# Optimization experiments

Hardware: AMD Instinct MI355X
Metric: run time of the kernel (lower is better)

Reference implementation:

```python
import jax, jax.numpy as jnp
import numpy as np

D_MODEL = 1024
N_HEADS = 16
D_K = D_MODEL // N_HEADS
FF_DIM = 4096
EPS = 1e-6
NEG = -1.0e9


def _layernorm(x, g, b):
    # torch: a_2 * (x - mean) / (std + eps) + b_2, std is unbiased (ddof=1)
    mean = jnp.mean(x, axis=-1, keepdims=True)
    std = jnp.std(x, axis=-1, keepdims=True, ddof=1)
    return g * (x - mean) / (std + EPS) + b


def setup_inputs() -> dict:
    key = jax.random.key(0)
    ks = jax.random.split(key, 8)
    s = 0.02
    x = jax.random.normal(ks[0], (2, 2048, D_MODEL), dtype=jnp.float32)
    mask = jnp.ones((2, 1, 1, 2048), dtype=jnp.int32)
    return {
        "x": x,
        "mask": mask,
        "wq": jax.random.normal(ks[1], (D_MODEL, D_MODEL), jnp.float32) * s,
        "wk": jax.random.normal(ks[2], (D_MODEL, D_MODEL), jnp.float32) * s,
        "wv": jax.random.normal(ks[3], (D_MODEL, D_MODEL), jnp.float32) * s,
        "wo": jax.random.normal(ks[4], (D_MODEL, D_MODEL), jnp.float32) * s,
        "bq": jnp.zeros((D_MODEL,), jnp.float32),
        "bk": jnp.zeros((D_MODEL,), jnp.float32),
        "bv": jnp.zeros((D_MODEL,), jnp.float32),
        "bo": jnp.zeros((D_MODEL,), jnp.float32),
        "w1": jax.random.normal(ks[5], (D_MODEL, FF_DIM), jnp.float32) * s,
        "b1": jnp.zeros((FF_DIM,), jnp.float32),
        "w2": jax.random.normal(ks[6], (FF_DIM, D_MODEL), jnp.float32) * s,
        "b2": jnp.zeros((D_MODEL,), jnp.float32),
        "ln1_g": jnp.ones((D_MODEL,), jnp.float32),
        "ln1_b": jnp.zeros((D_MODEL,), jnp.float32),
        "ln2_g": jnp.ones((D_MODEL,), jnp.float32),
        "ln2_b": jnp.zeros((D_MODEL,), jnp.float32),
    }


def reference(x, mask, wq, wk, wv, wo, bq, bk, bv, bo, w1, b1, w2, b2,
              ln1_g, ln1_b, ln2_g, ln2_b):
    B, S, _ = x.shape
    # --- sublayer 1: pre-norm self-attention with residual ---
    h = _layernorm(x, ln1_g, ln1_b)
    q = (h @ wq + bq).reshape(B, S, N_HEADS, D_K).transpose(0, 2, 1, 3)
    k = (h @ wk + bk).reshape(B, S, N_HEADS, D_K).transpose(0, 2, 1, 3)
    v = (h @ wv + bv).reshape(B, S, N_HEADS, D_K).transpose(0, 2, 1, 3)
    scores = jnp.einsum('bhqd,bhkd->bhqk', q, k) / np.sqrt(D_K).astype(np.float32)
    scores = jnp.where(mask == 0, NEG, scores)
    attn = jax.nn.softmax(scores, axis=-1)
    ctx = jnp.einsum('bhqk,bhkd->bhqd', attn, v)
    ctx = ctx.transpose(0, 2, 1, 3).reshape(B, S, D_MODEL)
    x = x + (ctx @ wo + bo)
    # --- sublayer 2: pre-norm FFN with residual ---
    h2 = _layernorm(x, ln2_g, ln2_b)
    ff = jax.nn.relu(h2 @ w1 + b1) @ w2 + b2
    return x + ff
```

## Files before the change

kernel.cpp:

```cpp
#include <hip/hip_runtime.h>

typedef unsigned short u16;
typedef unsigned int u32;
typedef __attribute__((ext_vector_type(8))) short bf16x8;
typedef __attribute__((ext_vector_type(4))) float f32x4;

__device__ __forceinline__ u16 f2bf(float f) {
  union { float f; unsigned int u; } x;
  x.f = f;
  unsigned int r = x.u + 0x7fffu + ((x.u >> 16) & 1u);
  return (u16)(r >> 16);
}

__device__ __forceinline__ float bf2f(u16 v) {
  union { unsigned int u; float f; } x;
  x.u = ((unsigned int)v) << 16;
  return x.f;
}

__device__ __forceinline__ u32 fbits(float f) {
  union { float f; u32 u; } x; x.f = f; return x.u;
}

__device__ __forceinline__ void async16(const u16* g, u16* l) {
  __builtin_amdgcn_global_load_lds((const __attribute__((address_space(1))) void*)g,
                                   (__attribute__((address_space(3))) void*)l, 16, 0, 0);
}

__device__ __forceinline__ void stage128x64(const u16* __restrict__ src, long row0, int k0,
                                            int ld, u16* lds, int wave, int lane) {
#pragma unroll
  for (int r = 0; r < 4; ++r) {
    int s = r * 256 + wave * 64 + lane;
    int row = s >> 3;
    int c = (s & 7) ^ (row & 7);
    async16(src + (row0 + row) * (long)ld + k0 + c * 8, lds + (r * 256 + wave * 64) * 8);
  }
}

__device__ __forceinline__ void stage64x128(const u16* __restrict__ src, int col0, int ld,
                                            u16* lds, int wave, int lane) {
#pragma unroll
  for (int r = 0; r < 4; ++r) {
    int s = r * 256 + wave * 64 + lane;
    int row = s >> 4;
    int c = (s & 15) ^ (row & 15);
    async16(src + (long)row * ld + col0 + c * 8, lds + (r * 256 + wave * 64) * 8);
  }
}

__device__ __forceinline__ void ln_core(float4 v, const float* g, const float* b, int t,
                                        u16* outrow) {
  float s = v.x + v.y + v.z + v.w;
  float ss = v.x * v.x + v.y * v.y + v.z * v.z + v.w * v.w;
#pragma unroll
  for (int off = 32; off; off >>= 1) {
    s += __shfl_xor(s, off);
    ss += __shfl_xor(ss, off);
  }
  __shared__ float red[8];
  int wave = t >> 6, lane = t & 63;
  if (lane == 0) { red[wave] = s; red[wave + 4] = ss; }
  __syncthreads();
  float tot = red[0] + red[1] + red[2] + red[3];
  float tots = red[4] + red[5] + red[6] + red[7];
  float mean = tot * (1.0f / 1024.0f);
  float var = (tots - 1024.0f * mean * mean) * (1.0f / 1023.0f);
  var = fmaxf(var, 0.0f);
  float inv = 1.0f / (sqrtf(var) + 1e-6f);
  float4 gv = ((const float4*)g)[t];
  float4 bv = ((const float4*)b)[t];
  union { unsigned long long u64; u16 h[4]; } o;
  o.h[0] = f2bf(gv.x * (v.x - mean) * inv + bv.x);
  o.h[1] = f2bf(gv.y * (v.y - mean) * inv + bv.y);
  o.h[2] = f2bf(gv.z * (v.z - mean) * inv + bv.z);
  o.h[3] = f2bf(gv.w * (v.w - mean) * inv + bv.w);
  *(unsigned long long*)(outrow + t * 4) = o.u64;
}

__global__ __launch_bounds__(256) void prep(const float* __restrict__ wq,
                                            const float* __restrict__ wk,
                                            const float* __restrict__ wv,
                                            const float* __restrict__ wo,
                                            const float* __restrict__ w1,
                                            const float* __restrict__ w2,
                                            const float* __restrict__ x,
                                            const float* __restrict__ ln1_g,
                                            const float* __restrict__ ln1_b,
                                            u16* __restrict__ wqkvT,
                                            u16* __restrict__ w1T,
                                            u16* __restrict__ w2T,
                                            u16* __restrict__ hout) {
  const int bid = blockIdx.x;
  const int part = bid >> 12;
  const int local = bid & 4095;
  const int t = threadIdx.x;
  if (part == 1) {
    float4 v = ((const float4*)(x + (long)local * 1024))[t];
    ln_core(v, ln1_g, ln1_b, t, hout + (long)local * 1024);
    return;
  }
  __shared__ float tile[32][33];
  const float* src; u16* dst; int C, R, bx, by;
  if (part == 0) {
    int sub = local >> 10;
    src = sub == 0 ? wq : (sub == 1 ? wk : (sub == 2 ? wv : wo));
    dst = wqkvT + (long)sub * 1024 * 1024;
    C = 1024; R = 1024; bx = local & 31; by = (local >> 5) & 31;
  } else if (part == 2) {
    src = w1; dst = w1T; C = 4096; R = 1024; bx = local & 127; by = local >> 7;
  } else {
    src = w2; dst = w2T; C = 1024; R = 4096; bx = local & 31; by = local >> 5;
  }
  int c0 = bx * 32, r0 = by * 32;
  int tx = t & 31, ty = t >> 5;
#pragma unroll
  for (int i = 0; i < 32; i += 8)
    tile[ty + i][tx] = src[(long)(r0 + ty + i) * C + c0 + tx];
  __syncthreads();
#pragma unroll
  for (int i = 0; i < 32; i += 8)
    dst[(long)(c0 + ty + i) * R + r0 + tx] = f2bf(tile[tx][ty + i]);
}

__global__ __launch_bounds__(256) void ln_fuse(const float* __restrict__ x,
                                               const float* __restrict__ bres,
                                               const u16* __restrict__ p0,
                                               const u16* __restrict__ p1,
                                               const float* __restrict__ g,
                                               const float* __restrict__ b,
                                               float* __restrict__ yout,
                                               u16* __restrict__ hout) {
  int row = blockIdx.x, t = threadIdx.x;
  long base = (long)row * 1024;
  float4 xv = ((const float4*)(x + base))[t];
  float4 bo = ((const float4*)bres)[t];
  ushort4 a = ((const ushort4*)(p0 + base))[t];
  ushort4 c = ((const ushort4*)(p1 + base))[t];
  float4 y;
  y.x = xv.x + bo.x + bf2f(a.x) + bf2f(c.x);
  y.y = xv.y + bo.y + bf2f(a.y) + bf2f(c.y);
  y.z = xv.z + bo.z + bf2f(a.z) + bf2f(c.z);
  y.w = xv.w + bo.w + bf2f(a.w) + bf2f(c.w);
  ((float4*)(yout + base))[t] = y;
  ln_core(y, g, b, t, hout + base);
}

__global__ __launch_bounds__(256) void final_add(float* __restrict__ out,
                                                 const float* __restrict__ b2,
                                                 const u16* __restrict__ p0,
                                                 const u16* __restrict__ p1) {
  int row = blockIdx.x, t = threadIdx.x;
  long base = (long)row * 1024;
  float4 o = ((float4*)(out + base))[t];
  float4 bb = ((const float4*)b2)[t];
  ushort4 a = ((const ushort4*)(p0 + base))[t];
  ushort4 c = ((const ushort4*)(p1 + base))[t];
  o.x += bb.x + bf2f(a.x) + bf2f(c.x);
  o.y += bb.y + bf2f(a.y) + bf2f(c.y);
  o.z += bb.z + bf2f(a.z) + bf2f(c.z);
  o.w += bb.w + bf2f(a.w) + bf2f(c.w);
  ((float4*)(out + base))[t] = o;
}

template <int MODE>
__global__ __launch_bounds__(256) void gemm_bt(const u16* __restrict__ A,
                                               const u16* __restrict__ Bt, int M, int N, int K,
                                               void* __restrict__ outp,
                                               const float* __restrict__ bias0,
                                               const float* __restrict__ bias1,
                                               const float* __restrict__ bias2,
                                               u16* __restrict__ q_out, u16* __restrict__ k_out,
                                               u16* __restrict__ v_out) {
  __shared__ __align__(16) u16 lds[17408];
  u16* ldsA = lds;
  u16* ldsB = lds + 8192;
  const int tid = threadIdx.x;
  const int wave = tid >> 6, lane = tid & 63;
  const int lane16 = lane & 15, quad = lane >> 4;
  const int wm = (wave >> 1) * 64, wn = (wave & 1) * 64;
  const long m0 = (long)blockIdx.y * 128;
  const long n0 = (long)blockIdx.x * 128;
  const int kLen = K / gridDim.z;
  const int kBeg = blockIdx.z * kLen;

  const f32x4 fzero = {0.f, 0.f, 0.f, 0.f};
  f32x4 acc[4][4];
#pragma unroll
  for (int i = 0; i < 4; ++i)
#pragma unroll
    for (int j = 0; j < 4; ++j) acc[i][j] = fzero;

  for (int k0 = kBeg; k0 < kBeg + kLen; k0 += 64) {
    stage128x64(A, m0, k0, K, ldsA, wave, lane);
    stage128x64(Bt, n0, k0, K, ldsB, wave, lane);
    __syncthreads();
#pragma unroll
    for (int kk = 0; kk < 2; ++kk) {
      bf16x8 af[4], bfr[4];
#pragma unroll
      for (int i = 0; i < 4; ++i) {
        int row = wm + i * 16 + lane16;
        int c = (kk * 4 + quad) ^ (row & 7);
        af[i] = *(const bf16x8*)(ldsA + row * 64 + c * 8);
      }
#pragma unroll
      for (int j = 0; j < 4; ++j) {
        int row = wn + j * 16 + lane16;
        int c = (kk * 4 + quad) ^ (row & 7);
        bfr[j] = *(const bf16x8*)(ldsB + row * 64 + c * 8);
      }
#pragma unroll
      for (int i = 0; i < 4; ++i)
#pragma unroll
        for (int j = 0; j < 4; ++j)
          acc[i][j] = __builtin_amdgcn_mfma_f32_16x16x32_bf16(af[i], bfr[j], acc[i][j], 0, 0, 0);
    }
    __syncthreads();
  }

  if (MODE == 0 && (int)(n0 >> 10) == 2) {
#pragma unroll
    for (int j = 0; j < 4; ++j) {
      int lcol = wn + j * 16 + lane16;
      float bvj = bias2[(int)(n0 - 2048) + lcol];
#pragma unroll
      for (int i = 0; i < 4; ++i)
#pragma unroll
        for (int r = 0; r < 4; ++r) {
          int lrow = wm + i * 16 + quad * 4 + r;
          lds[lcol * 136 + lrow] = f2bf(acc[i][j][r] + bvj);
        }
    }
    __syncthreads();
    int lcol = tid >> 1, seg = tid & 1;
    int cc = (int)(n0 - 2048) + lcol;
    int head = cc >> 6, d = cc & 63;
    int bI = (int)(m0 >> 11), s0 = (int)(m0 & 2047);
    u16* dst = v_out + ((long)(bI * 16 + head) * 64 + d) * 2048 + s0 + seg * 64;
    const u16* s = lds + lcol * 136 + seg * 64;
#pragma unroll
    for (int c2 = 0; c2 < 8; ++c2) ((uint4*)dst)[c2] = ((const uint4*)s)[c2];
    return;
  }

  u16* pp = nullptr;
  if (MODE == 1) pp = blockIdx.z == 0 ? (u16*)outp : q_out;

#pragma unroll
  for (int j = 0; j < 4; ++j) {
    int col = (int)n0 + wn + j * 16 + lane16;
#pragma unroll
    for (int i = 0; i < 4; ++i) {
#pragma unroll
      for (int r = 0; r < 4; ++r) {
        int row = (int)m0 + wm + i * 16 + quad * 4 + r;
        float val = acc[i][j][r];
        if (MODE == 0) {
          int which = col >> 10, cc = col & 1023;
          float vv = val + (which == 0 ? bias0[cc] : bias1[cc]);
          int bb = row >> 11, sS = row & 2047, head = cc >> 6, d = cc & 63;
          long bh = (long)bb * 16 + head;
          if (which == 0) {
            q_out[(bh * 2048 + sS) * 64 + d] = f2bf(vv * 0.18033688f);
          } else {
            k_out[(bh * 2048 + sS) * 64 + d] = f2bf(vv);
          }
        } else if (MODE == 1) {
          pp[(long)row * N + col] = f2bf(val);
        } else if (MODE == 2) {
          ((u16*)outp)[(long)row * N + col] = f2bf(fmaxf(val + bias0[col], 0.0f));
        }
      }
    }
  }
}

#define FA_C0 28.854239f
__global__ __launch_bounds__(256) void flash_attn(const u16* __restrict__ q,
                                                  const u16* __restrict__ k,
                                                  const u16* __restrict__ v,
                                                  const int* __restrict__ mask,
                                                  u16* __restrict__ ctx) {
  const int fid = blockIdx.y * 16 + blockIdx.x;
  const int xcd = fid & 7, slot = fid >> 3;
  const int bh = xcd * 4 + (slot >> 4);
  const int q0 = (slot & 15) * 128;
  const int b = bh >> 4, h = bh & 15;
  const int tid = threadIdx.x;
  const int wave = tid >> 6, lane = tid & 63;
  const int lane16 = lane & 15, quad = lane >> 4;

  const u16* qp = q + (long)bh * 2048 * 64;
  const u16* kp = k + (long)bh * 2048 * 64;
  const u16* vp = v + (long)bh * 64 * 2048;
  const int* mp = mask + b * 2048;

  __shared__ __align__(16) u16 ldsK[128 * 64];
  __shared__ __align__(16) u16 ldsVT[64 * 128];
  __shared__ __align__(16) u16 ldsP23[2 * 4096];
  __shared__ __align__(16) float ldsMask[128];
  __shared__ int ldsFlag[2];
  u16* myP = (wave < 2) ? (ldsK + wave * 4096) : (ldsP23 + (wave - 2) * 4096);

  bf16x8 qf[2][2];
#pragma unroll
  for (int g = 0; g < 2; ++g) {
    const long qrow = q0 + wave * 32 + g * 16 + lane16;
    qf[g][0] = *(const bf16x8*)(qp + qrow * 64 + quad * 8);
    qf[g][1] = *(const bf16x8*)(qp + qrow * 64 + 32 + quad * 8);
  }

  const f32x4 fzero = {0.f, 0.f, 0.f, 0.f};
  const f32x4 cC0 = {-FA_C0, -FA_C0, -FA_C0, -FA_C0};
  float l_loc[2] = {0.f, 0.f};
  f32x4 o_acc[2][4];
#pragma unroll
  for (int g = 0; g < 2; ++g)
#pragma unroll
    for (int j = 0; j < 4; ++j) o_acc[g][j] = fzero;

  const int xorm = (lane16 & 7) << 2;
  u16* const pw0 = myP + lane16 * 128;
  u16* const pw1 = myP + (16 + lane16) * 128;

  for (int kt = 0; kt < 2048; kt += 128) {
    stage128x64(kp, kt, 0, 64, ldsK, wave, lane);
    stage64x128(vp, kt, 2048, ldsVT, wave, lane);
    if (tid < 128) {
      int mv = mp[kt + tid];
      ldsMask[tid] = (mv == 0) ? -1.0e9f : 0.0f;
      unsigned long long bal = __ballot(mv != 0);
      if ((tid & 63) == 0) ldsFlag[tid >> 6] = (bal == ~0ull) ? 1 : 0;
    }
    __syncthreads();
    const bool allv = (ldsFlag[0] & ldsFlag[1]) != 0;

    f32x4 s_acc[8][2];
#pragma unroll
    for (int j = 0; j < 8; ++j) {
      int row = j * 16 + lane16;
      int c0i = quad ^ (row & 7);
      int c1i = (4 + quad) ^ (row & 7);
      bf16x8 kf0 = *(const bf16x8*)(ldsK + row * 64 + c0i * 8);
      bf16x8 kf1 = *(const bf16x8*)(ldsK + row * 64 + c1i * 8);
#pragma unroll
      for (int g = 0; g < 2; ++g) {
        f32x4 sa = __builtin_amdgcn_mfma_f32_16x16x32_bf16(kf0, qf[g][0], cC0, 0, 0, 0);
        sa = __builtin_amdgcn_mfma_f32_16x16x32_bf16(kf1, qf[g][1], sa, 0, 0, 0);
        s_acc[j][g] = sa;
      }
    }
    __syncthreads();

#pragma unroll
    for (int j = 0; j < 8; ++j) {
      int cw = ((4 * j + quad) ^ xorm) * 4;
#pragma unroll
      for (int g = 0; g < 2; ++g) {
        f32x4 sa = s_acc[j][g];
        if (!allv) {
          f32x4 mk = *(const f32x4*)(ldsMask + j * 16 + quad * 4);
          sa = sa + mk;
        }
        float p0 = __builtin_exp2f(sa[0]);
        float p1 = __builtin_exp2f(sa[1]);
        float p2 = __builtin_exp2f(sa[2]);
        float p3 = __builtin_exp2f(sa[3]);
        l_loc[g] += (p0 + p1) + (p2 + p3);
        uint2 pk;
        pk.x = __builtin_amdgcn_perm(fbits(p1), fbits(p0), 0x07060302u);
        pk.y = __builtin_amdgcn_perm(fbits(p3), fbits(p2), 0x07060302u);
        *(uint2*)((g ? pw1 : pw0) + cw) = pk;
      }
    }
#pragma unroll
    for (int kk = 0; kk < 4; ++kk) {
      int cr = ((8 * kk + 2 * quad) ^ xorm) * 4;
      bf16x8 pf0 = *(const bf16x8*)(pw0 + cr);
      bf16x8 pf1 = *(const bf16x8*)(pw1 + cr);
#pragma unroll
      for (int jj = 0; jj < 4; ++jj) {
        int row = jj * 16 + lane16;
        int cv = (kk * 4 + quad) ^ (row & 15);
        bf16x8 vf = *(const bf16x8*)(ldsVT + row * 128 + cv * 8);
        o_acc[0][jj] = __builtin_amdgcn_mfma_f32_16x16x32_bf16(pf0, vf, o_acc[0][jj], 0, 0, 0);
        o_acc[1][jj] = __builtin_amdgcn_mfma_f32_16x16x32_bf16(pf1, vf, o_acc[1][jj], 0, 0, 0);
      }
    }
    __syncthreads();
  }

  float lr[2][4];
#pragma unroll
  for (int g = 0; g < 2; ++g) {
    float l = l_loc[g];
#pragma unroll
    for (int off = 16; off < 64; off <<= 1) l += __shfl_xor(l, off);
    float linv = 1.0f / l;
#pragma unroll
    for (int r = 0; r < 4; ++r) lr[g][r] = __shfl(linv, quad * 4 + r);
  }

#pragma unroll
  for (int g = 0; g < 2; ++g)
#pragma unroll
    for (int jj = 0; jj < 4; ++jj)
#pragma unroll
      for (int r = 0; r < 4; ++r) {
        int sg = q0 + wave * 32 + g * 16 + quad * 4 + r;
        int d = jj * 16 + lane16;
        float val = o_acc[g][jj][r] * lr[g][r];
        ctx[((long)b * 2048 + sg) * 1024 + h * 64 + d] = f2bf(val);
      }
}

extern "C" void kernel_launch(void* const* d_in, const int* in_sizes, int n_in, void* d_out,
                              int out_size, void* d_ws, size_t ws_size, hipStream_t stream) {
  (void)in_sizes; (void)n_in; (void)out_size; (void)ws_size;
  const float* x  = (const float*)d_in[0];
  const int* mask = (const int*)d_in[1];
  const float* wq = (const float*)d_in[2];
  const float* wk = (const float*)d_in[3];
  const float* wv = (const float*)d_in[4];
  const float* wo = (const float*)d_in[5];
  const float* bq = (const float*)d_in[6];
  const float* bk = (const float*)d_in[7];
  const float* bv = (const float*)d_in[8];
  const float* bo = (const float*)d_in[9];
  const float* w1 = (const float*)d_in[10];
  const float* b1 = (const float*)d_in[11];
  const float* w2 = (const float*)d_in[12];
  const float* b2 = (const float*)d_in[13];
  const float* ln1_g = (const float*)d_in[14];
  const float* ln1_b = (const float*)d_in[15];
  const float* ln2_g = (const float*)d_in[16];
  const float* ln2_b = (const float*)d_in[17];
  float* out = (float*)d_out;

  u16* ws = (u16*)d_ws;
  u16* wqkvT = ws;
  u16* woT = wqkvT + 3072 * 1024;
  u16* w1T = woT + 1024 * 1024;
  u16* w2T = w1T + 4096 * 1024;
  u16* h   = w2T + 4096 * 1024;
  u16* qb  = h + 4096 * 1024;
  u16* kb  = qb + 4096 * 1024;
  u16* vb  = kb + 4096 * 1024;
  u16* ctx = vb + 4096 * 1024;
  u16* ffh = qb;
  u16* f2p0 = ws;
  u16* f2p1 = w1T;

  prep<<<16384, 256, 0, stream>>>(wq, wk, wv, wo, w1, w2, x, ln1_g, ln1_b,
                                  wqkvT, w1T, w2T, h);

  gemm_bt<0><<<dim3(24, 32), 256, 0, stream>>>(h, wqkvT, 4096, 3072, 1024, nullptr, bq, bk, bv,
                                               qb, kb, vb);

  flash_attn<<<dim3(16, 32), 256, 0, stream>>>(qb, kb, vb, mask, ctx);

  gemm_bt<1><<<dim3(8, 32, 2), 256, 0, stream>>>(ctx, woT, 4096, 1024, 1024, qb, nullptr,
                                                 nullptr, nullptr, kb, nullptr, nullptr);

  ln_fuse<<<4096, 256, 0, stream>>>(x, bo, qb, kb, ln2_g, ln2_b, out, h);

  gemm_bt<2><<<dim3(32, 32), 256, 0, stream>>>(h, w1T, 4096, 4096, 1024, ffh, b1, nullptr,
                                               nullptr, nullptr, nullptr, nullptr);

  gemm_bt<1><<<dim3(8, 32, 2), 256, 0, stream>>>(ffh, w2T, 4096, 1024, 4096, f2p0, nullptr,
                                                 nullptr, nullptr, f2p1, nullptr, nullptr);

  final_add<<<4096, 256, 0, stream>>>(out, b2, f2p0, f2p1);
}
```

Measured before the change: 363.4 us.

## Use 256x256 8-wave pipelined GEMM for FFN and atomic split-K output

Adds a new 512-thread GEMM kernel with 256x256 tiles, a double-buffered LDS pipeline that stages half-tiles interleaved with MFMA phases, and priority hints. It replaces the two FFN GEMMs. The second GEMM now uses 4-way split-K and atomically adds its partials plus bias straight into the fp32 output, which removes the separate bf16 partial buffers and the final_add kernel. In exchange it uses a large LDS footprint at one block per CU, and the fp32 atomics make the summation order nondeterministic.

```diff
diff --git a/kernel.cpp b/kernel.cpp
--- a/kernel.cpp
+++ b/kernel.cpp
@@ -35,6 +35,17 @@
     int row = s >> 3;
     int c = (s & 7) ^ (row & 7);
     async16(src + (row0 + row) * (long)ld + k0 + c * 8, lds + (r * 256 + wave * 64) * 8);
+  }
+}
+
+__device__ __forceinline__ void stage_half512(const u16* __restrict__ src, long row0, int k0,
+                                              int ld, u16* lbase, int wave, int lane) {
+#pragma unroll
+  for (int r = 0; r < 2; ++r) {
+    int s = r * 512 + wave * 64 + lane;
+    int row = s >> 3;
+    int c = (s & 7) ^ (row & 7);
+    async16(src + (row0 + row) * (long)ld + k0 + c * 8, lbase + (r * 512 + wave * 64) * 8);
   }
 }
 
@@ -146,23 +157,6 @@
   ln_core(y, g, b, t, hout + base);
 }
 
-__global__ __launch_bounds__(256) void final_add(float* __restrict__ out,
-                                                 const float* __restrict__ b2,
-                                                 const u16* __restrict__ p0,
-                                                 const u16* __restrict__ p1) {
-  int row = blockIdx.x, t = threadIdx.x;
-  long base = (long)row * 1024;
-  float4 o = ((float4*)(out + base))[t];
-  float4 bb = ((const float4*)b2)[t];
-  ushort4 a = ((const ushort4*)(p0 + base))[t];
-  ushort4 c = ((const ushort4*)(p1 + base))[t];
-  o.x += bb.x + bf2f(a.x) + bf2f(c.x);
-  o.y += bb.y + bf2f(a.y) + bf2f(c.y);
-  o.z += bb.z + bf2f(a.z) + bf2f(c.z);
-  o.w += bb.w + bf2f(a.w) + bf2f(c.w);
-  ((float4*)(out + base))[t] = o;
-}
-
 template <int MODE>
 __global__ __launch_bounds__(256) void gemm_bt(const u16* __restrict__ A,
                                                const u16* __restrict__ Bt, int M, int N, int K,
@@ -268,9 +262,175 @@
           }
         } else if (MODE == 1) {
           pp[(long)row * N + col] = f2bf(val);
-        } else if (MODE == 2) {
-          ((u16*)outp)[(long)row * N + col] = f2bf(fmaxf(val + bias0[col], 0.0f));
         }
+      }
+    }
+  }
+}
+
+template <int MODE>
+__global__ __launch_bounds__(512, 1) void gemm8(const u16* __restrict__ A,
+                                                const u16* __restrict__ Bt, int M, int N, int K,
+                                                void* __restrict__ outp,
+                                                const float* __restrict__ bias) {
+  __shared__ __align__(16) u16 lds[65536];
+  (void)M;
+  const int tid = threadIdx.x;
+  const int wave = tid >> 6, lane = tid & 63;
+  const int lane16 = lane & 15, quad = lane >> 4;
+  const int wr = wave >> 2, wc = wave & 3;
+  const long m0 = (long)blockIdx.y * 256;
+  const long n0 = (long)blockIdx.x * 256;
+  const int kLen = K / gridDim.z;
+  const int kBeg = blockIdx.z * kLen;
+  const int nT = kLen >> 6;
+
+  u16* const ldsA = lds;
+  u16* const ldsB = lds + 32768;
+
+  const f32x4 fzero = {0.f, 0.f, 0.f, 0.f};
+  f32x4 acc[8][4];
+#pragma unroll
+  for (int m = 0; m < 8; ++m)
+#pragma unroll
+    for (int n = 0; n < 4; ++n) acc[m][n] = fzero;
+
+  stage_half512(Bt, n0,       kBeg,      K, ldsB,         wave, lane);
+  stage_half512(A,  m0,       kBeg,      K, ldsA,         wave, lane);
+  stage_half512(Bt, n0 + 128, kBeg,      K, ldsB + 8192,  wave, lane);
+  stage_half512(A,  m0 + 128, kBeg,      K, ldsA + 8192,  wave, lane);
+  stage_half512(Bt, n0,       kBeg + 64, K, ldsB + 16384, wave, lane);
+  stage_half512(A,  m0,       kBeg + 64, K, ldsA + 16384, wave, lane);
+  asm volatile("s_waitcnt vmcnt(4)" ::: "memory");
+  asm volatile("s_barrier" ::: "memory");
+
+  for (int t = 0; t < nT; ++t) {
+    u16* const aB = ldsA + (t & 1) * 16384;
+    u16* const bB = ldsB + (t & 1) * 16384;
+    u16* const aN1 = ldsA + ((t + 1) & 1) * 16384;
+    u16* const bN1 = ldsB + ((t + 1) & 1) * 16384;
+    const int k1 = kBeg + (t + 1 < nT ? t + 1 : nT - 1) * 64;
+    const int k2 = kBeg + (t + 2 < nT ? t + 2 : nT - 1) * 64;
+
+    bf16x8 af[4][2], bf01[2][2], bf23[2][2];
+
+#pragma unroll
+    for (int m = 0; m < 4; ++m) {
+      const int row = wr * 128 + m * 16 + lane16;
+#pragma unroll
+      for (int kk = 0; kk < 2; ++kk)
+        af[m][kk] = *(const bf16x8*)(aB + row * 64 + (((kk * 4 + quad) ^ (row & 7)) << 3));
+    }
+#pragma unroll
+    for (int n = 0; n < 2; ++n) {
+      const int row = wc * 64 + n * 16 + lane16;
+#pragma unroll
+      for (int kk = 0; kk < 2; ++kk)
+        bf01[n][kk] = *(const bf16x8*)(bB + row * 64 + (((kk * 4 + quad) ^ (row & 7)) << 3));
+    }
+    stage_half512(Bt, n0 + 128, k1, K, bN1 + 8192, wave, lane);
+    asm volatile("s_barrier" ::: "memory");
+    asm volatile("s_waitcnt lgkmcnt(0)" ::: "memory");
+    __builtin_amdgcn_sched_barrier(0);
+    __builtin_amdgcn_s_setprio(1);
+#pragma unroll
+    for (int m = 0; m < 4; ++m)
+#pragma unroll
+      for (int n = 0; n < 2; ++n) {
+        acc[m][n] = __builtin_amdgcn_mfma_f32_16x16x32_bf16(af[m][0], bf01[n][0], acc[m][n], 0, 0, 0);
+        acc[m][n] = __builtin_amdgcn_mfma_f32_16x16x32_bf16(af[m][1], bf01[n][1], acc[m][n], 0, 0, 0);
+      }
+    __builtin_amdgcn_s_setprio(0);
+    asm volatile("s_barrier" ::: "memory");
+
+#pragma unroll
+    for (int n = 0; n < 2; ++n) {
+      const int row = wc * 64 + (n + 2) * 16 + lane16;
+#pragma unroll
+      for (int kk = 0; kk < 2; ++kk)
+        bf23[n][kk] = *(const bf16x8*)(bB + row * 64 + (((kk * 4 + quad) ^ (row & 7)) << 3));
+    }
+    stage_half512(A, m0 + 128, k1, K, aN1 + 8192, wave, lane);
+    asm volatile("s_barrier" ::: "memory");
+    asm volatile("s_waitcnt lgkmcnt(0)" ::: "memory");
+    __builtin_amdgcn_sched_barrier(0);
+    __builtin_amdgcn_s_setprio(1);
+#pragma unroll
+    for (int m = 0; m < 4; ++m)
+#pragma unroll
+      for (int n = 0; n < 2; ++n) {
+        acc[m][n + 2] = __builtin_amdgcn_mfma_f32_16x16x32_bf16(af[m][0], bf23[n][0], acc[m][n + 2], 0, 0, 0);
+        acc[m][n + 2] = __builtin_amdgcn_mfma_f32_16x16x32_bf16(af[m][1], bf23[n][1], acc[m][n + 2], 0, 0, 0);
+      }
+    __builtin_amdgcn_s_setprio(0);
+    asm volatile("s_barrier" ::: "memory");
+
+#pragma unroll
+    for (int m = 0; m < 4; ++m) {
+      const int row = wr * 128 + (m + 4) * 16 + lane16;
+#pragma unroll
+      for (int kk = 0; kk < 2; ++kk)
+        af[m][kk] = *(const bf16x8*)(aB + row * 64 + (((kk * 4 + quad) ^ (row & 7)) << 3));
+    }
+    stage_half512(Bt, n0, k2, K, bB, wave, lane);
+    asm volatile("s_barrier" ::: "memory");
+    asm volatile("s_waitcnt lgkmcnt(0)" ::: "memory");
+    __builtin_amdgcn_sched_barrier(0);
+    __builtin_amdgcn_s_setprio(1);
+#pragma unroll
+    for (int m = 0; m < 4; ++m)
+#pragma unroll
+      for (int n = 0; n < 2; ++n) {
+        acc[m + 4][n + 2] = __builtin_amdgcn_mfma_f32_16x16x32_bf16(af[m][0], bf23[n][0], acc[m + 4][n + 2], 0, 0, 0);
+        acc[m + 4][n + 2] = __builtin_amdgcn_mfma_f32_16x16x32_bf16(af[m][1], bf23[n][1], acc[m + 4][n + 2], 0, 0, 0);
+      }
+    __builtin_amdgcn_s_setprio(0);
+    asm volatile("s_barrier" ::: "memory");
+
+    stage_half512(A, m0, k2, K, aB, wave, lane);
+    asm volatile("s_barrier" ::: "memory");
+    __builtin_amdgcn_s_setprio(1);
+#pragma unroll
+    for (int m = 0; m < 4; ++m)
+#pragma unroll
+      for (int n = 0; n < 2; ++n) {
+        acc[m + 4][n] = __builtin_amdgcn_mfma_f32_16x16x32_bf16(af[m][0], bf01[n][0], acc[m + 4][n], 0, 0, 0);
+        acc[m + 4][n] = __builtin_amdgcn_mfma_f32_16x16x32_bf16(af[m][1], bf01[n][1], acc[m + 4][n], 0, 0, 0);
+      }
+    __builtin_amdgcn_s_setprio(0);
+    asm volatile("s_waitcnt vmcnt(4)" ::: "memory");
+    asm volatile("s_barrier" ::: "memory");
+  }
+
+  asm volatile("s_waitcnt vmcnt(0)" ::: "memory");
+
+  if (MODE == 2) {
+    u16* op = (u16*)outp;
+#pragma unroll
+    for (int n = 0; n < 4; ++n) {
+      const int col = (int)n0 + wc * 64 + n * 16 + lane16;
+      const float bv = bias[col];
+#pragma unroll
+      for (int m = 0; m < 8; ++m) {
+        const long rbase = ((long)m0 + wr * 128 + m * 16 + quad * 4) * N + col;
+#pragma unroll
+        for (int r = 0; r < 4; ++r)
+          op[rbase + (long)r * N] = f2bf(fmaxf(acc[m][n][r] + bv, 0.0f));
+      }
+    }
+  } else {
+    float* op = (float*)outp;
+    const bool z0 = (blockIdx.z == 0);
+#pragma unroll
+    for (int n = 0; n < 4; ++n) {
+      const int col = (int)n0 + wc * 64 + n * 16 + lane16;
+      const float bv = z0 ? bias[col] : 0.0f;
+#pragma unroll
+      for (int m = 0; m < 8; ++m) {
+        const long rbase = ((long)m0 + wr * 128 + m * 16 + quad * 4) * N + col;
+#pragma unroll
+        for (int r = 0; r < 4; ++r)
+          unsafeAtomicAdd(op + rbase + (long)r * N, acc[m][n][r] + bv);
       }
     }
   }
@@ -449,8 +609,6 @@
   u16* vb  = kb + 4096 * 1024;
   u16* ctx = vb + 4096 * 1024;
   u16* ffh = qb;
-  u16* f2p0 = ws;
-  u16* f2p1 = w1T;
 
   prep<<<16384, 256, 0, stream>>>(wq, wk, wv, wo, w1, w2, x, ln1_g, ln1_b,
                                   wqkvT, w1T, w2T, h);
@@ -465,11 +623,7 @@
 
   ln_fuse<<<4096, 256, 0, stream>>>(x, bo, qb, kb, ln2_g, ln2_b, out, h);
 
-  gemm_bt<2><<<dim3(32, 32), 256, 0, stream>>>(h, w1T, 4096, 4096, 1024, ffh, b1, nullptr,
-                                               nullptr, nullptr, nullptr, nullptr);
-
-  gemm_bt<1><<<dim3(8, 32, 2), 256, 0, stream>>>(ffh, w2T, 4096, 1024, 4096, f2p0, nullptr,
-                                                 nullptr, nullptr, f2p1, nullptr, nullptr);
-
-  final_add<<<4096, 256, 0, stream>>>(out, b2, f2p0, f2p1);
-}
+  gemm8<2><<<dim3(16, 16), 512, 0, stream>>>(h, w1T, 4096, 4096, 1024, ffh, b1);
+
+  gemm8<1><<<dim3(4, 16, 4), 512, 0, stream>>>(ffh, w2T, 4096, 1024, 4096, out, b2);
+}
```

After: 383.4 us. 5.5% more time.
